# Kernel optimization log

Hardware: AMD Instinct MI355X
Metric: run time of the kernel (lower is better)

## Reference

```python
import jax, jax.numpy as jnp
import numpy as np

B, H, W, IN_C = 2, 64, 64, 3
D = 192            # embed_dim
DEPTH = 4
DI = 2 * D         # d_inner (mamba expand=2)
DS = 16            # d_state
DC = 4             # d_conv
DTR = -(-D // 16)  # dt_rank = ceil(D/16) = 12
EPS = 1e-5


def setup_inputs() -> dict:
    key = jax.random.key(0)
    ks = jax.random.split(key, 8)
    def rn(k, shape, s=0.02):
        return jax.random.normal(k, shape, dtype=jnp.float32) * s
    x = jax.random.normal(ks[0], (B, IN_C, H, W), dtype=jnp.float32)
    proj_w = rn(ks[1], (D, IN_C))
    proj_b = jnp.zeros((D,), jnp.float32)
    lp_w = rn(ks[2], (DEPTH, D, 2 * D))          # linear_proj: (out=D, in=2D)
    lp_b = jnp.zeros((DEPTH, D), jnp.float32)
    norm_w = jnp.ones((DEPTH, D), jnp.float32)
    in_w = rn(ks[3], (DEPTH, 2 * DI, D))         # mamba in_proj (no bias)
    conv_w = rn(ks[4], (DEPTH, DI, DC), 0.1)     # depthwise causal conv1d
    conv_b = jnp.zeros((DEPTH, DI), jnp.float32)
    xproj_w = rn(ks[5], (DEPTH, DTR + 2 * DS, DI))
    dt_w = rn(ks[6], (DEPTH, DI, DTR), 0.1)
    dt0 = np.random.default_rng(0).uniform(1e-3, 0.1, size=(DEPTH, DI)).astype(np.float32)
    dt_b = jnp.asarray(np.log(np.expm1(dt0)))    # softplus-inverse init (mamba default)
    A_log = jnp.tile(jnp.log(jnp.arange(1, DS + 1, dtype=jnp.float32)), (DEPTH, DI, 1))
    Dp = jnp.ones((DEPTH, DI), jnp.float32)
    out_w = rn(ks[7], (DEPTH, D, DI))
    normf_w = jnp.ones((D,), jnp.float32)
    return dict(x=x, proj_w=proj_w, proj_b=proj_b, lp_w=lp_w, lp_b=lp_b,
                norm_w=norm_w, in_w=in_w, conv_w=conv_w, conv_b=conv_b,
                xproj_w=xproj_w, dt_w=dt_w, dt_b=dt_b, A_log=A_log, Dp=Dp,
                out_w=out_w, normf_w=normf_w)


def _rmsnorm(x, w):
    return x * jax.lax.rsqrt(jnp.mean(x * x, axis=-1, keepdims=True) + EPS) * w


def _mamba(x, in_w, conv_w, conv_b, xproj_w, dt_w, dt_b, A_log, Dp, out_w):
    # x: (B, N, D)
    Bsz = x.shape[0]
    xz = jnp.einsum('bnd,ed->bne', x, in_w)                 # (B,N,2*DI)
    xi, z = jnp.split(xz, 2, axis=-1)
    # causal depthwise conv1d along sequence (pad left d_conv-1)
    xt = xi.transpose(0, 2, 1)                              # (B,DI,N)
    xc = jax.lax.conv_general_dilated(xt, conv_w[:, None, :], (1,), [(DC - 1, 0)],
                                      feature_group_count=DI)
    xi = jax.nn.silu((xc + conv_b[None, :, None]).transpose(0, 2, 1))  # (B,N,DI)
    dbc = jnp.einsum('bni,ei->bne', xi, xproj_w)            # (B,N,DTR+2*DS)
    dt = jax.nn.softplus(jnp.einsum('bnr,ir->bni', dbc[..., :DTR], dt_w) + dt_b)
    Bm = dbc[..., DTR:DTR + DS]                             # (B,N,DS)
    Cm = dbc[..., DTR + DS:]                                # (B,N,DS)
    A = -jnp.exp(A_log)                                     # (DI,DS)
    dA = jnp.exp(dt[..., None] * A)                         # (B,N,DI,DS)
    dBx = dt[..., None] * Bm[:, :, None, :] * xi[..., None] # (B,N,DI,DS)
    def step(h, inp):
        a, bx = inp
        h = a * h + bx
        return h, h
    h0 = jnp.zeros((Bsz, DI, DS), x.dtype)
    _, hs = jax.lax.scan(step, h0, (dA.transpose(1, 0, 2, 3), dBx.transpose(1, 0, 2, 3)))
    y = jnp.einsum('nbis,bns->bni', hs, Cm) + Dp * xi
    y = y * jax.nn.silu(z)
    return jnp.einsum('bni,di->bnd', y, out_w)


def _block(x, lp_w, lp_b, norm_w, mp):
    # DeltaVisionMambaBlock: token-diff -> linear_proj -> RMSNorm -> Mamba -> +skip
    prev = jnp.concatenate([jnp.zeros_like(x[:, :1]), x[:, :-1]], axis=1)
    comb = jnp.concatenate([x, x - prev], axis=-1)          # (B,N,2D)
    proj = jnp.einsum('bnc,dc->bnd', comb, lp_w) + lp_b
    return _mamba(_rmsnorm(proj, norm_w), *mp) + x


def reference(x, proj_w, proj_b, lp_w, lp_b, norm_w, in_w, conv_w, conv_b,
              xproj_w, dt_w, dt_b, A_log, Dp, out_w, normf_w):
    Bsz = x.shape[0]
    feat = jnp.einsum('bchw,dc->bdhw', x, proj_w) + proj_b[None, :, None, None]
    seq = feat.reshape(Bsz, D, H * W).transpose(0, 2, 1)    # (B,N,D)
    for l in range(DEPTH):
        mp = (in_w[l], conv_w[l], conv_b[l], xproj_w[l], dt_w[l], dt_b[l],
              A_log[l], Dp[l], out_w[l])
        seq = _block(seq, lp_w[l], lp_b[l], norm_w[l], mp)
    seq = _rmsnorm(seq, normf_w)
    return seq.transpose(0, 2, 1).reshape(Bsz, D, H, W)
```

## Files before the change

kernel.cpp:

```cpp
#include <hip/hip_runtime.h>
#include <hip/hip_bf16.h>

#define BB 2
#define NN 4096
#define DD 192
#define DI 384
#define DS 16
#define DTR 12
#define DC 4
#define DEPTH 4
#define NT (BB*NN)
#define NCH 128
#define CL 32
#define EPSF 1e-5f

#define OFF_X       0
#define OFF_PROJ_W  24576
#define OFF_PROJ_B  25152
#define OFF_LP_W    25344
#define OFF_LP_B    320256
#define OFF_NORM_W  321024
#define OFF_IN_W    321792
#define OFF_CONV_W  911616
#define OFF_CONV_B  917760
#define OFF_XPROJ_W 919296
#define OFF_DT_W    986880
#define OFF_DT_B    1005312
#define OFF_A_LOG   1006848
#define OFF_DP      1031424
#define OFF_OUT_W   1032960
#define OFF_NORMF_W 1327872
#define ARENA_TOTAL 1328064
#define ARENA_BYTES 2656160

typedef __hip_bfloat16 bf16_t;
typedef unsigned short u16;
typedef unsigned int u32;
typedef __attribute__((ext_vector_type(8))) unsigned short u16x8;
typedef __attribute__((ext_vector_type(8))) short s16x8;
typedef __attribute__((ext_vector_type(4))) float f32x4;

struct Ptrs { const void* p[16]; };

__device__ __forceinline__ float bf(u16 v){ return __uint_as_float(((u32)v)<<16); }
__device__ __forceinline__ u16 f2bf(float f){
  u32 b = __float_as_uint(f);
  return (u16)((b + 0x7FFFu + ((b>>16)&1u)) >> 16);
}

__global__ __launch_bounds__(256) void k_detect(const u16* __restrict__ x, int* flag){
  __shared__ int cnt;
  if (threadIdx.x==0) cnt=0;
  __syncthreads();
  u32 v = x[2*threadIdx.x];
  int ex = (int)((v>>7)&0xFF);
  if (ex>=100 && ex<=140) atomicAdd(&cnt,1);
  __syncthreads();
  if (threadIdx.x==0) *flag = (cnt>128) ? 0 : 1;
}

__global__ __launch_bounds__(256) void k_cvt(Ptrs ps, const int* __restrict__ flag, u16* __restrict__ arena){
  int e = blockIdx.x*256 + threadIdx.x;
  if (e >= ARENA_TOTAL) return;
  const void* sp; int off;
  if      (e < OFF_PROJ_W ){ sp=ps.p[0];  off=OFF_X; }
  else if (e < OFF_PROJ_B ){ sp=ps.p[1];  off=OFF_PROJ_W; }
  else if (e < OFF_LP_W   ){ sp=ps.p[2];  off=OFF_PROJ_B; }
  else if (e < OFF_LP_B   ){ sp=ps.p[3];  off=OFF_LP_W; }
  else if (e < OFF_NORM_W ){ sp=ps.p[4];  off=OFF_LP_B; }
  else if (e < OFF_IN_W   ){ sp=ps.p[5];  off=OFF_NORM_W; }
  else if (e < OFF_CONV_W ){ sp=ps.p[6];  off=OFF_IN_W; }
  else if (e < OFF_CONV_B ){ sp=ps.p[7];  off=OFF_CONV_W; }
  else if (e < OFF_XPROJ_W){ sp=ps.p[8];  off=OFF_CONV_B; }
  else if (e < OFF_DT_W   ){ sp=ps.p[9];  off=OFF_XPROJ_W; }
  else if (e < OFF_DT_B   ){ sp=ps.p[10]; off=OFF_DT_W; }
  else if (e < OFF_A_LOG  ){ sp=ps.p[11]; off=OFF_DT_B; }
  else if (e < OFF_DP     ){ sp=ps.p[12]; off=OFF_A_LOG; }
  else if (e < OFF_OUT_W  ){ sp=ps.p[13]; off=OFF_DP; }
  else if (e < OFF_NORMF_W){ sp=ps.p[14]; off=OFF_OUT_W; }
  else                     { sp=ps.p[15]; off=OFF_NORMF_W; }
  int k = e - off;
  if (*flag){
    u32 v = ((const u32*)sp)[k];
    arena[e] = (u16)((v + 0x7FFFu + ((v>>16)&1u)) >> 16);
  } else {
    arena[e] = ((const u16*)sp)[k];
  }
}

__global__ __launch_bounds__(256) void k_proj(const u16* __restrict__ x, const u16* __restrict__ pw,
                                              const u16* __restrict__ pb, float* __restrict__ seq){
  int idx = blockIdx.x*256 + threadIdx.x;
  if (idx >= NT*DD) return;
  int d = idx % DD; int bn = idx / DD; int b = bn >> 12; int n = bn & (NN-1);
  float acc = bf(pb[d]);
  acc += bf(x[(b*3+0)*NN + n]) * bf(pw[d*3+0]);
  acc += bf(x[(b*3+1)*NN + n]) * bf(pw[d*3+1]);
  acc += bf(x[(b*3+2)*NN + n]) * bf(pw[d*3+2]);
  seq[idx] = acc;
}

__global__ __launch_bounds__(256) void k_lp_norm(const float* __restrict__ seq,
    const u16* __restrict__ lp_w, const u16* __restrict__ lp_b, const u16* __restrict__ norm_w,
    u16* __restrict__ xn){
  const int tid = threadIdx.x;
  const int n0 = blockIdx.x*16;
  __shared__ u16 combL[16][392];
  __shared__ u16 wL[192][72];
  __shared__ float accL[16][200];
  __shared__ float ssq[16];
  const int w = tid>>6, lane = tid&63, lm = lane&15, lk = lane>>4;

  for (int idx = tid*4; idx < 16*DD; idx += 1024){
    int t = idx/DD, d = idx%DD;
    int gn = n0 + t;
    float4 cur = *(const float4*)&seq[gn*DD + d];
    float4 prv = make_float4(0.f,0.f,0.f,0.f);
    if ((gn & (NN-1)) != 0) prv = *(const float4*)&seq[(gn-1)*DD + d];
    combL[t][d+0]=f2bf(cur.x); combL[t][d+1]=f2bf(cur.y); combL[t][d+2]=f2bf(cur.z); combL[t][d+3]=f2bf(cur.w);
    combL[t][DD+d+0]=f2bf(cur.x-prv.x); combL[t][DD+d+1]=f2bf(cur.y-prv.y);
    combL[t][DD+d+2]=f2bf(cur.z-prv.z); combL[t][DD+d+3]=f2bf(cur.w-prv.w);
  }
  f32x4 acc[3];
  #pragma unroll
  for (int i=0;i<3;++i) acc[i] = (f32x4){0.f,0.f,0.f,0.f};
  for (int c=0;c<6;++c){
    for (int idx = tid*8; idx < 192*64; idx += 2048){
      int row = idx >> 6, col = idx & 63;
      *(u16x8*)&wL[row][col] = *(const u16x8*)(lp_w + row*384 + c*64 + col);
    }
    __syncthreads();
    #pragma unroll
    for (int ks=0; ks<2; ++ks){
      s16x8 a = *(s16x8*)&combL[lm][c*64 + ks*32 + lk*8];
      #pragma unroll
      for (int nt=0; nt<3; ++nt){
        s16x8 b = *(s16x8*)&wL[(w*3+nt)*16 + lm][ks*32 + lk*8];
        acc[nt] = __builtin_amdgcn_mfma_f32_16x16x32_bf16(a, b, acc[nt], 0, 0, 0);
      }
    }
    __syncthreads();
  }
  #pragma unroll
  for (int nt=0; nt<3; ++nt)
    #pragma unroll
    for (int r=0; r<4; ++r){
      int m = lk*4 + r;
      int n = (w*3+nt)*16 + lm;
      accL[m][n] = acc[nt][r] + bf(lp_b[n]);
    }
  __syncthreads();
  {
    int tok = tid >> 4, j = tid & 15;
    float s = 0.f;
    #pragma unroll
    for (int c2=0;c2<12;++c2){ float v = accL[tok][j*12+c2]; s += v*v; }
    s += __shfl_xor(s,1); s += __shfl_xor(s,2); s += __shfl_xor(s,4); s += __shfl_xor(s,8);
    if (j==0) ssq[tok] = rsqrtf(s*(1.f/DD) + EPSF);
  }
  __syncthreads();
  for (int idx = tid; idx < 16*DD; idx += 256){
    int t = idx/DD, d = idx%DD;
    xn[(n0+t)*DD + d] = f2bf(accL[t][d] * ssq[t] * bf(norm_w[d]));
  }
}

__global__ __launch_bounds__(256) void k_inproj(const u16* __restrict__ xn,
    const u16* __restrict__ in_w, u16* __restrict__ xi_c, u16* __restrict__ zz_b){
  const int tid = threadIdx.x;
  const int m0 = blockIdx.x*64;
  const int e0 = blockIdx.y*64;
  __shared__ u16 aL[64][200];
  __shared__ u16 bL[64][200];
  for (int idx = tid*8; idx < 64*192; idx += 2048){
    int row = idx/192, col = idx%192;
    *(u16x8*)&aL[row][col] = *(const u16x8*)(xn   + (m0+row)*192 + col);
    *(u16x8*)&bL[row][col] = *(const u16x8*)(in_w + (e0+row)*192 + col);
  }
  __syncthreads();
  const int w = tid >> 6, lane = tid & 63;
  const int lm = lane & 15, lk = lane >> 4;
  f32x4 acc[4];
  #pragma unroll
  for (int i=0;i<4;++i) acc[i] = (f32x4){0.f,0.f,0.f,0.f};
  #pragma unroll
  for (int ks=0; ks<6; ++ks){
    s16x8 a = *(s16x8*)&aL[w*16 + lm][ks*32 + lk*8];
    #pragma unroll
    for (int nt=0; nt<4; ++nt){
      s16x8 b = *(s16x8*)&bL[nt*16 + lm][ks*32 + lk*8];
      acc[nt] = __builtin_amdgcn_mfma_f32_16x16x32_bf16(a, b, acc[nt], 0, 0, 0);
    }
  }
  #pragma unroll
  for (int nt=0; nt<4; ++nt){
    int e = e0 + nt*16 + lm;
    #pragma unroll
    for (int r=0; r<4; ++r){
      int tok = m0 + w*16 + lk*4 + r;
      u16 v = f2bf(acc[nt][r]);
      if (e0 < DI) xi_c[tok*DI + e]      = v;
      else         zz_b[tok*DI + e - DI] = v;
    }
  }
}

__global__ __launch_bounds__(256) void k_xproj_dt(const u16* __restrict__ xi_c,
    const u16* __restrict__ conv_w, const u16* __restrict__ conv_b,
    const u16* __restrict__ xproj_w, const u16* __restrict__ dt_w, const u16* __restrict__ dt_bv,
    u16* __restrict__ xc_g, float* __restrict__ dt_o, float* __restrict__ Bm, float* __restrict__ Cm){
  const int tid = threadIdx.x;
  const int n0 = blockIdx.x*16;
  const int basei = n0 & ~(NN-1);
  __shared__ u16 xcL[16][392];
  __shared__ u16 dtwL[384][24];
  __shared__ float dbcL[16][16];
  ((float*)dbcL)[tid] = 0.f;
  for (int idx=tid*8; idx<16*384; idx+=2048){
    int r=idx/384, c=idx%384;
    int gn = n0 + r;
    float vals[4][8];
    #pragma unroll
    for (int q=0;q<4;++q){
      int row = gn-3+q;
      if (row >= basei){
        u16x8 xv = *(const u16x8*)(xi_c + row*DI + c);
        #pragma unroll
        for (int j=0;j<8;++j) vals[q][j] = bf(xv[j]);
      } else {
        #pragma unroll
        for (int j=0;j<8;++j) vals[q][j] = 0.f;
      }
    }
    u16x8 cw0 = *(const u16x8*)(conv_w + c*4);
    u16x8 cw1 = *(const u16x8*)(conv_w + c*4 + 8);
    u16x8 cw2 = *(const u16x8*)(conv_w + c*4 + 16);
    u16x8 cw3 = *(const u16x8*)(conv_w + c*4 + 24);
    u16x8 cb  = *(const u16x8*)(conv_b + c);
    u16x8 ov;
    #pragma unroll
    for (int j=0;j<8;++j){
      u16 cwa, cwb, cwc, cwd;
      int jj = j*4;
      if (jj < 8)       { cwa=cw0[jj];    cwb=cw0[jj+1];  cwc=cw0[jj+2];  cwd=cw0[jj+3]; }
      else if (jj < 16) { cwa=cw1[jj-8];  cwb=cw1[jj-7];  cwc=cw1[jj-6];  cwd=cw1[jj-5]; }
      else if (jj < 24) { cwa=cw2[jj-16]; cwb=cw2[jj-15]; cwc=cw2[jj-14]; cwd=cw2[jj-13]; }
      else              { cwa=cw3[jj-24]; cwb=cw3[jj-23]; cwc=cw3[jj-22]; cwd=cw3[jj-21]; }
      float acc = bf(cb[j]) + vals[0][j]*bf(cwa) + vals[1][j]*bf(cwb) + vals[2][j]*bf(cwc) + vals[3][j]*bf(cwd);
      float v = acc/(1.f+__expf(-acc));
      ov[j] = f2bf(v);
    }
    *(u16x8*)&xcL[r][c] = ov;
    *(u16x8*)(xc_g + gn*DI + c) = ov;
  }
  for (int idx=tid; idx<384*12; idx+=256){
    int r2=idx/12, c2=idx%12;
    dtwL[r2][c2] = dt_w[idx];
    dtwL[r2][12+c2] = 0;
  }
  __syncthreads();
  const int w = tid>>6, lane = tid&63, lm = lane&15, lk = lane>>4;
  const s16x8 zb = {0,0,0,0,0,0,0,0};
  if (w < 3){
    f32x4 acc = {0.f,0.f,0.f,0.f};
    #pragma unroll
    for (int ks=0; ks<12; ++ks){
      s16x8 a = *(s16x8*)&xcL[lm][ks*32 + lk*8];
      s16x8 b = (w < 2 || lm < 12) ? *(const s16x8*)(xproj_w + (w*16+lm)*384 + ks*32 + lk*8) : zb;
      acc = __builtin_amdgcn_mfma_f32_16x16x32_bf16(a, b, acc, 0, 0, 0);
    }
    int e = w*16 + lm;
    #pragma unroll
    for (int r=0;r<4;++r){
      int m = lk*4 + r;
      int gm = n0 + m;
      if      (e < 12) dbcL[m][e] = acc[r];
      else if (e < 28) Bm[gm*DS + e-12] = acc[r];
      else if (e < 44) Cm[gm*DS + e-28] = acc[r];
    }
  }
  __syncthreads();
  s16x8 a_dt = zb;
  if (lk < 2){
    #pragma unroll
    for (int j=0;j<8;++j) a_dt[j] = (short)f2bf(dbcL[lm][lk*8+j]);
  }
  #pragma unroll
  for (int q=0;q<6;++q){
    int nt = w*6 + q;
    s16x8 b = (lk<2) ? *(s16x8*)&dtwL[nt*16+lm][lk*8] : zb;
    f32x4 acc = {0.f,0.f,0.f,0.f};
    acc = __builtin_amdgcn_mfma_f32_16x16x32_bf16(a_dt, b, acc, 0, 0, 0);
    int i = nt*16 + lm;
    float bias = bf(dt_bv[i]);
    #pragma unroll
    for (int r=0;r<4;++r){
      int m = lk*4 + r;
      float xval = acc[r] + bias;
      float sp = (xval>20.f)? xval : log1pf(__expf(xval));
      dt_o[(n0+m)*DI + i] = sp;
    }
  }
}

__global__ __launch_bounds__(128) void k_scan1(const float* __restrict__ dt,
    const u16* __restrict__ xc, const float* __restrict__ Bm, const u16* __restrict__ A_log,
    float* __restrict__ P, float* __restrict__ Q){
  const int tid = threadIdx.x;
  const int i = blockIdx.x*128 + tid;
  const int ch = blockIdx.y, b = blockIdx.z;
  __shared__ float bm_l[CL][DS];
  {
    int r = tid>>2, c4 = (tid&3)*4;
    *(float4*)&bm_l[r][c4] = *(const float4*)&Bm[(b*NN + ch*CL + r)*DS + c4];
  }
  float Av[DS];
  {
    u16x8 a0 = *(const u16x8*)(A_log + i*DS);
    u16x8 a1 = *(const u16x8*)(A_log + i*DS + 8);
    #pragma unroll
    for (int s=0;s<8;++s){ Av[s] = -__expf(bf(a0[s])); Av[8+s] = -__expf(bf(a1[s])); }
  }
  __syncthreads();
  float Pv[DS], h[DS];
  #pragma unroll
  for (int s=0;s<DS;++s){ Pv[s]=1.f; h[s]=0.f; }
  const int nb = b*NN + ch*CL;
  #pragma unroll 4
  for (int t=0;t<CL;++t){
    float xv  = bf(xc[(nb+t)*DI + i]);
    float dtv = dt[(nb+t)*DI + i];
    float dtx = dtv*xv;
    #pragma unroll
    for (int s=0;s<DS;++s){
      float a = __expf(dtv*Av[s]);
      Pv[s] *= a;
      h[s] = a*h[s] + dtx*bm_l[t][s];
    }
  }
  const int base = ((b*DI + i)*NCH + ch)*DS;
  #pragma unroll
  for (int s4=0;s4<4;++s4){
    *(float4*)&P[base+s4*4] = make_float4(Pv[s4*4+0],Pv[s4*4+1],Pv[s4*4+2],Pv[s4*4+3]);
    *(float4*)&Q[base+s4*4] = make_float4(h[s4*4+0],h[s4*4+1],h[s4*4+2],h[s4*4+3]);
  }
}

__global__ __launch_bounds__(256) void k_scan2(const float* __restrict__ P, const float* __restrict__ Q,
                                               float* __restrict__ Hin){
  int tid = blockIdx.x*256 + threadIdx.x;
  int s = tid & 15; int ci = tid >> 4;
  float h = 0.f;
  for (int ch=0; ch<NCH; ++ch){
    int idx = (ci*NCH+ch)*DS + s;
    Hin[idx] = h;
    h = P[idx]*h + Q[idx];
  }
}

__global__ __launch_bounds__(128) void k_scan3(const float* __restrict__ dt,
    const u16* __restrict__ xc, const float* __restrict__ Bm, const float* __restrict__ Cm,
    const u16* __restrict__ zz_b, const u16* __restrict__ A_log, const u16* __restrict__ Dp,
    const float* __restrict__ Hin, u16* __restrict__ Y){
  const int tid = threadIdx.x;
  const int i = blockIdx.x*128 + tid;
  const int ch = blockIdx.y, b = blockIdx.z;
  __shared__ float bm_l[CL][DS], cm_l[CL][DS];
  {
    int r = tid>>2, c4 = (tid&3)*4;
    *(float4*)&bm_l[r][c4] = *(const float4*)&Bm[(b*NN + ch*CL + r)*DS + c4];
    *(float4*)&cm_l[r][c4] = *(const float4*)&Cm[(b*NN + ch*CL + r)*DS + c4];
  }
  float Av[DS];
  {
    u16x8 a0 = *(const u16x8*)(A_log + i*DS);
    u16x8 a1 = *(const u16x8*)(A_log + i*DS + 8);
    #pragma unroll
    for (int s=0;s<8;++s){ Av[s] = -__expf(bf(a0[s])); Av[8+s] = -__expf(bf(a1[s])); }
  }
  const float Dv = bf(Dp[i]);
  float h[DS];
  const int base = ((b*DI + i)*NCH + ch)*DS;
  #pragma unroll
  for (int s4=0;s4<4;++s4){
    float4 hv = *(const float4*)&Hin[base+s4*4];
    h[s4*4+0]=hv.x; h[s4*4+1]=hv.y; h[s4*4+2]=hv.z; h[s4*4+3]=hv.w;
  }
  __syncthreads();
  const int nb = b*NN + ch*CL;
  #pragma unroll 4
  for (int t=0;t<CL;++t){
    float xv  = bf(xc[(nb+t)*DI + i]);
    float dtv = dt[(nb+t)*DI + i];
    float zv  = bf(zz_b[(nb+t)*DI + i]);
    float dtx = dtv*xv;
    float y = 0.f;
    #pragma unroll
    for (int s=0;s<DS;++s){
      float a = __expf(dtv*Av[s]);
      h[s] = a*h[s] + dtx*bm_l[t][s];
      y += h[s]*cm_l[t][s];
    }
    y += Dv*xv;
    y *= zv/(1.f+__expf(-zv));
    Y[(nb+t)*DI + i] = f2bf(y);
  }
}

__global__ __launch_bounds__(256) void k_out(const u16* __restrict__ Y,
    const u16* __restrict__ out_w, float* __restrict__ seq){
  const int tid = threadIdx.x;
  const int m0 = blockIdx.x*64;
  const int d0 = blockIdx.y*64;
  __shared__ u16 aL[64][200];
  __shared__ u16 bL[64][200];
  const int w = tid >> 6, lane = tid & 63;
  const int lm = lane & 15, lk = lane >> 4;
  f32x4 acc[4];
  #pragma unroll
  for (int i=0;i<4;++i) acc[i] = (f32x4){0.f,0.f,0.f,0.f};
  for (int c=0; c<2; ++c){
    const int kc = c*192;
    for (int idx = tid*8; idx < 64*192; idx += 2048){
      int row = idx/192, col = idx%192;
      *(u16x8*)&aL[row][col] = *(const u16x8*)(Y     + (m0+row)*DI + kc + col);
      *(u16x8*)&bL[row][col] = *(const u16x8*)(out_w + (d0+row)*DI + kc + col);
    }
    __syncthreads();
    #pragma unroll
    for (int ks=0; ks<6; ++ks){
      s16x8 a = *(s16x8*)&aL[w*16 + lm][ks*32 + lk*8];
      #pragma unroll
      for (int nt=0; nt<4; ++nt){
        s16x8 b = *(s16x8*)&bL[nt*16 + lm][ks*32 + lk*8];
        acc[nt] = __builtin_amdgcn_mfma_f32_16x16x32_bf16(a, b, acc[nt], 0, 0, 0);
      }
    }
    __syncthreads();
  }
  #pragma unroll
  for (int nt=0; nt<4; ++nt){
    int d = d0 + nt*16 + lm;
    #pragma unroll
    for (int r=0; r<4; ++r){
      int tok = m0 + w*16 + lk*4 + r;
      seq[tok*DD + d] += acc[nt][r];
    }
  }
}

__global__ __launch_bounds__(192) void k_final(const float* __restrict__ seq,
    const u16* __restrict__ normf_w, void* __restrict__ out, const int* __restrict__ flag){
  const int d = threadIdx.x;
  const int bn = blockIdx.x;
  const int b = bn >> 12, n = bn & (NN-1);
  __shared__ float wred[3];
  float v = seq[bn*DD + d];
  float s = v*v;
  #pragma unroll
  for (int off=32; off>=1; off>>=1) s += __shfl_down(s,off);
  if ((d&63)==0) wred[d>>6]=s;
  __syncthreads();
  float r = rsqrtf((wred[0]+wred[1]+wred[2])*(1.f/DD) + EPSF);
  float res = v * r * bf(normf_w[d]);
  int o = (b*DD+d)*NN + n;
  if (*flag) ((float*)out)[o] = res;
  else       ((u16*)out)[o]   = f2bf(res);
}

extern "C" void kernel_launch(void* const* d_in, const int* in_sizes, int n_in,
                              void* d_out, int out_size, void* d_ws, size_t ws_size,
                              hipStream_t stream){
  Ptrs ps;
  for (int i=0;i<16;++i) ps.p[i] = d_in[i];

  u16* arena = (u16*)d_ws;
  int* flag  = (int*)((char*)d_ws + ARENA_TOTAL*2);
  float* fbase = (float*)((char*)d_ws + ARENA_BYTES);

  float* seq  = fbase;
  float* dt   = seq  + NT*DD;
  float* Bm   = dt   + NT*DI;
  float* Cm   = Bm   + NT*DS;
  float* Hin  = Cm   + NT*DS;
  float* Pb   = Hin  + BB*DI*NCH*DS;
  float* Qb   = Pb   + BB*DI*NCH*DS;
  u16* xn_b   = (u16*)(Qb + BB*DI*NCH*DS);
  u16* xi_c   = xn_b + NT*DD;
  u16* zz_b   = xi_c + NT*DI;
  u16* Y_b    = zz_b + NT*DI;
  u16* xc_b   = Y_b  + NT*DI;

  const u16* xA      = arena + OFF_X;
  const u16* proj_w  = arena + OFF_PROJ_W;
  const u16* proj_b  = arena + OFF_PROJ_B;
  const u16* lp_w    = arena + OFF_LP_W;
  const u16* lp_b    = arena + OFF_LP_B;
  const u16* norm_w  = arena + OFF_NORM_W;
  const u16* in_w    = arena + OFF_IN_W;
  const u16* conv_w  = arena + OFF_CONV_W;
  const u16* conv_b  = arena + OFF_CONV_B;
  const u16* xproj_w = arena + OFF_XPROJ_W;
  const u16* dt_w    = arena + OFF_DT_W;
  const u16* dt_b    = arena + OFF_DT_B;
  const u16* A_log   = arena + OFF_A_LOG;
  const u16* Dp      = arena + OFF_DP;
  const u16* out_w   = arena + OFF_OUT_W;
  const u16* normf_w = arena + OFF_NORMF_W;

  k_detect<<<1, 256, 0, stream>>>((const u16*)d_in[0], flag);
  k_cvt<<<(ARENA_TOTAL+255)/256, 256, 0, stream>>>(ps, flag, arena);

  k_proj<<<(NT*DD+255)/256, 256, 0, stream>>>(xA, proj_w, proj_b, seq);
  for (int l=0; l<DEPTH; ++l){
    k_lp_norm<<<NT/16, 256, 0, stream>>>(seq, lp_w + l*DD*2*DD, lp_b + l*DD, norm_w + l*DD, xn_b);
    k_inproj<<<dim3(NT/64, 12), 256, 0, stream>>>(xn_b, in_w + l*2*DI*DD, xi_c, zz_b);
    k_xproj_dt<<<NT/16, 256, 0, stream>>>(xi_c, conv_w + l*DI*DC, conv_b + l*DI,
        xproj_w + l*(DTR+2*DS)*DI, dt_w + l*DI*DTR, dt_b + l*DI, xc_b, dt, Bm, Cm);
    k_scan1<<<dim3(DI/128, NCH, BB), 128, 0, stream>>>(dt, xc_b, Bm, A_log + l*DI*DS, Pb, Qb);
    k_scan2<<<(BB*DI*DS)/256, 256, 0, stream>>>(Pb, Qb, Hin);
    k_scan3<<<dim3(DI/128, NCH, BB), 128, 0, stream>>>(dt, xc_b, Bm, Cm, zz_b,
        A_log + l*DI*DS, Dp + l*DI, Hin, Y_b);
    k_out<<<dim3(NT/64, 3), 256, 0, stream>>>(Y_b, out_w + l*DD*DI, seq);
  }
  k_final<<<NT, 192, 0, stream>>>(seq, normf_w, d_out, flag);
}
```

Baseline: 606.4 us.

## Fuse chunk-local scan pass into xproj/dt kernel with 16-token chunks

Merges the first scan pass (per-chunk decay product and local state) into the conv/xproj/dt kernel, so each 16-token block computes chunk P/Q straight from shared memory instead of re-reading dt, xc and B from global memory in a separate launch. To match the 16-token block, the chunk length is halved and the chunk count doubled, which doubles the sequential length of the cross-chunk scan2 loop and the P/Q/Hin traffic. It also adds about 25KB of shared memory per block and serialises the scan work over 256 threads for 384 channels, which may reduce occupancy.

```diff
diff --git a/kernel.cpp b/kernel.cpp
--- a/kernel.cpp
+++ b/kernel.cpp
@@ -10,8 +10,8 @@
 #define DC 4
 #define DEPTH 4
 #define NT (BB*NN)
-#define NCH 128
-#define CL 32
+#define NCH 256
+#define CL 16
 #define EPSF 1e-5f
 
 #define OFF_X       0
@@ -205,16 +205,22 @@
   }
 }
 
-__global__ __launch_bounds__(256) void k_xproj_dt(const u16* __restrict__ xi_c,
+__global__ __launch_bounds__(256) void k_xds(const u16* __restrict__ xi_c,
     const u16* __restrict__ conv_w, const u16* __restrict__ conv_b,
     const u16* __restrict__ xproj_w, const u16* __restrict__ dt_w, const u16* __restrict__ dt_bv,
-    u16* __restrict__ xc_g, float* __restrict__ dt_o, float* __restrict__ Bm, float* __restrict__ Cm){
+    const u16* __restrict__ A_log,
+    u16* __restrict__ xc_g, float* __restrict__ dt_g, float* __restrict__ Bm, float* __restrict__ Cm,
+    float* __restrict__ P, float* __restrict__ Q){
   const int tid = threadIdx.x;
   const int n0 = blockIdx.x*16;
   const int basei = n0 & ~(NN-1);
+  const int b = n0 >> 12;
+  const int ch = (n0 & (NN-1)) >> 4;
   __shared__ u16 xcL[16][392];
+  __shared__ float dtL[16][388];
   __shared__ u16 dtwL[384][24];
   __shared__ float dbcL[16][16];
+  __shared__ float bmL[16][16];
   ((float*)dbcL)[tid] = 0.f;
   for (int idx=tid*8; idx<16*384; idx+=2048){
     int r=idx/384, c=idx%384;
@@ -266,8 +272,8 @@
     #pragma unroll
     for (int ks=0; ks<12; ++ks){
       s16x8 a = *(s16x8*)&xcL[lm][ks*32 + lk*8];
-      s16x8 b = (w < 2 || lm < 12) ? *(const s16x8*)(xproj_w + (w*16+lm)*384 + ks*32 + lk*8) : zb;
-      acc = __builtin_amdgcn_mfma_f32_16x16x32_bf16(a, b, acc, 0, 0, 0);
+      s16x8 bb = (w < 2 || lm < 12) ? *(const s16x8*)(xproj_w + (w*16+lm)*384 + ks*32 + lk*8) : zb;
+      acc = __builtin_amdgcn_mfma_f32_16x16x32_bf16(a, bb, acc, 0, 0, 0);
     }
     int e = w*16 + lm;
     #pragma unroll
@@ -275,7 +281,7 @@
       int m = lk*4 + r;
       int gm = n0 + m;
       if      (e < 12) dbcL[m][e] = acc[r];
-      else if (e < 28) Bm[gm*DS + e-12] = acc[r];
+      else if (e < 28){ Bm[gm*DS + e-12] = acc[r]; bmL[m][e-12] = acc[r]; }
       else if (e < 44) Cm[gm*DS + e-28] = acc[r];
     }
   }
@@ -288,9 +294,9 @@
   #pragma unroll
   for (int q=0;q<6;++q){
     int nt = w*6 + q;
-    s16x8 b = (lk<2) ? *(s16x8*)&dtwL[nt*16+lm][lk*8] : zb;
+    s16x8 bb = (lk<2) ? *(s16x8*)&dtwL[nt*16+lm][lk*8] : zb;
     f32x4 acc = {0.f,0.f,0.f,0.f};
-    acc = __builtin_amdgcn_mfma_f32_16x16x32_bf16(a_dt, b, acc, 0, 0, 0);
+    acc = __builtin_amdgcn_mfma_f32_16x16x32_bf16(a_dt, bb, acc, 0, 0, 0);
     int i = nt*16 + lm;
     float bias = bf(dt_bv[i]);
     #pragma unroll
@@ -298,51 +304,42 @@
       int m = lk*4 + r;
       float xval = acc[r] + bias;
       float sp = (xval>20.f)? xval : log1pf(__expf(xval));
-      dt_o[(n0+m)*DI + i] = sp;
-    }
-  }
-}
-
-__global__ __launch_bounds__(128) void k_scan1(const float* __restrict__ dt,
-    const u16* __restrict__ xc, const float* __restrict__ Bm, const u16* __restrict__ A_log,
-    float* __restrict__ P, float* __restrict__ Q){
-  const int tid = threadIdx.x;
-  const int i = blockIdx.x*128 + tid;
-  const int ch = blockIdx.y, b = blockIdx.z;
-  __shared__ float bm_l[CL][DS];
-  {
-    int r = tid>>2, c4 = (tid&3)*4;
-    *(float4*)&bm_l[r][c4] = *(const float4*)&Bm[(b*NN + ch*CL + r)*DS + c4];
-  }
-  float Av[DS];
-  {
-    u16x8 a0 = *(const u16x8*)(A_log + i*DS);
-    u16x8 a1 = *(const u16x8*)(A_log + i*DS + 8);
-    #pragma unroll
-    for (int s=0;s<8;++s){ Av[s] = -__expf(bf(a0[s])); Av[8+s] = -__expf(bf(a1[s])); }
-  }
-  __syncthreads();
-  float Pv[DS], h[DS];
-  #pragma unroll
-  for (int s=0;s<DS;++s){ Pv[s]=1.f; h[s]=0.f; }
-  const int nb = b*NN + ch*CL;
-  #pragma unroll 4
-  for (int t=0;t<CL;++t){
-    float xv  = bf(xc[(nb+t)*DI + i]);
-    float dtv = dt[(nb+t)*DI + i];
-    float dtx = dtv*xv;
-    #pragma unroll
-    for (int s=0;s<DS;++s){
-      float a = __expf(dtv*Av[s]);
-      Pv[s] *= a;
-      h[s] = a*h[s] + dtx*bm_l[t][s];
-    }
-  }
-  const int base = ((b*DI + i)*NCH + ch)*DS;
-  #pragma unroll
-  for (int s4=0;s4<4;++s4){
-    *(float4*)&P[base+s4*4] = make_float4(Pv[s4*4+0],Pv[s4*4+1],Pv[s4*4+2],Pv[s4*4+3]);
-    *(float4*)&Q[base+s4*4] = make_float4(h[s4*4+0],h[s4*4+1],h[s4*4+2],h[s4*4+3]);
+      dtL[m][i] = sp;
+      dt_g[(n0+m)*DI + i] = sp;
+    }
+  }
+  __syncthreads();
+  for (int cc=0; cc<2; ++cc){
+    int i = tid + cc*256;
+    if (i >= DI) break;
+    float Av[DS];
+    {
+      u16x8 a0 = *(const u16x8*)(A_log + i*DS);
+      u16x8 a1 = *(const u16x8*)(A_log + i*DS + 8);
+      #pragma unroll
+      for (int s=0;s<8;++s){ Av[s] = -__expf(bf(a0[s])); Av[8+s] = -__expf(bf(a1[s])); }
+    }
+    float Pv[DS], h[DS];
+    #pragma unroll
+    for (int s=0;s<DS;++s){ Pv[s]=1.f; h[s]=0.f; }
+    #pragma unroll 4
+    for (int t=0;t<CL;++t){
+      float dtv = dtL[t][i];
+      float xv  = bf(xcL[t][i]);
+      float dtx = dtv*xv;
+      #pragma unroll
+      for (int s=0;s<DS;++s){
+        float a = __expf(dtv*Av[s]);
+        Pv[s] *= a;
+        h[s] = a*h[s] + dtx*bmL[t][s];
+      }
+    }
+    const int base = ((b*DI + i)*NCH + ch)*DS;
+    #pragma unroll
+    for (int s4=0;s4<4;++s4){
+      *(float4*)&P[base+s4*4] = make_float4(Pv[s4*4+0],Pv[s4*4+1],Pv[s4*4+2],Pv[s4*4+3]);
+      *(float4*)&Q[base+s4*4] = make_float4(h[s4*4+0],h[s4*4+1],h[s4*4+2],h[s4*4+3]);
+    }
   }
 }
 
@@ -367,9 +364,9 @@
   const int ch = blockIdx.y, b = blockIdx.z;
   __shared__ float bm_l[CL][DS], cm_l[CL][DS];
   {
-    int r = tid>>2, c4 = (tid&3)*4;
-    *(float4*)&bm_l[r][c4] = *(const float4*)&Bm[(b*NN + ch*CL + r)*DS + c4];
-    *(float4*)&cm_l[r][c4] = *(const float4*)&Cm[(b*NN + ch*CL + r)*DS + c4];
+    int r = (tid>>2)&15, c4 = (tid&3)*4;
+    if (tid < 64)       *(float4*)&bm_l[r][c4] = *(const float4*)&Bm[(b*NN + ch*CL + r)*DS + c4];
+    else                *(float4*)&cm_l[r][c4] = *(const float4*)&Cm[(b*NN + ch*CL + r)*DS + c4];
   }
   float Av[DS];
   {
@@ -515,9 +512,9 @@
   for (int l=0; l<DEPTH; ++l){
     k_lp_norm<<<NT/16, 256, 0, stream>>>(seq, lp_w + l*DD*2*DD, lp_b + l*DD, norm_w + l*DD, xn_b);
     k_inproj<<<dim3(NT/64, 12), 256, 0, stream>>>(xn_b, in_w + l*2*DI*DD, xi_c, zz_b);
-    k_xproj_dt<<<NT/16, 256, 0, stream>>>(xi_c, conv_w + l*DI*DC, conv_b + l*DI,
-        xproj_w + l*(DTR+2*DS)*DI, dt_w + l*DI*DTR, dt_b + l*DI, xc_b, dt, Bm, Cm);
-    k_scan1<<<dim3(DI/128, NCH, BB), 128, 0, stream>>>(dt, xc_b, Bm, A_log + l*DI*DS, Pb, Qb);
+    k_xds<<<NT/16, 256, 0, stream>>>(xi_c, conv_w + l*DI*DC, conv_b + l*DI,
+        xproj_w + l*(DTR+2*DS)*DI, dt_w + l*DI*DTR, dt_b + l*DI, A_log + l*DI*DS,
+        xc_b, dt, Bm, Cm, Pb, Qb);
     k_scan2<<<(BB*DI*DS)/256, 256, 0, stream>>>(Pb, Qb, Hin);
     k_scan3<<<dim3(DI/128, NCH, BB), 128, 0, stream>>>(dt, xc_b, Bm, Cm, zz_b,
         A_log + l*DI*DS, Dp + l*DI, Hin, Y_b);
```

Measured after the change: 557.7 us. 1.09x faster.
